# Kernel optimization log

Measured on AMD Instinct MI355X. Metric: run time of the kernel, lower is better.

The kernel has to match this reference:

```python
import math
import jax, jax.numpy as jnp
import numpy as np

B, CK, CV, T, H, W = 4, 512, 512, 3, 24, 24


def _conv(x, w, b):
    # 3x3, stride 1, pad 1 == SAME
    y = jax.lax.conv_general_dilated(x, w, (1, 1), 'SAME',
                                     dimension_numbers=('NCHW', 'OIHW', 'NCHW'))
    return y + b[None, :, None, None]


def _resblock(x, c1w, c1b, c2w, c2b, dsw=None, dsb=None):
    r = _conv(jax.nn.relu(x), c1w, c1b)
    r = _conv(jax.nn.relu(r), c2w, c2b)
    s = x if dsw is None else _conv(x, dsw, dsb)
    return s + r


def _up2(x):
    b, c, h, w = x.shape
    return jax.image.resize(x, (b, c, 2 * h, 2 * w), 'bilinear')


def _affinity(mk, qk):
    # mk: [B,CK,T,H,W], qk: [B,CK,H,W]
    b, ck = mk.shape[:2]
    mkf = mk.reshape(b, ck, -1)                       # [B,CK,THW]
    qkf = qk.reshape(b, ck, -1)                       # [B,CK,HW]
    a = jnp.sum(mkf * mkf, axis=1)[:, :, None]        # [B,THW,1]
    ab = 2.0 * jnp.einsum('bct,bcn->btn', mkf, qkf)   # [B,THW,HW]
    return jax.nn.softmax((-a + ab) / math.sqrt(ck), axis=1)


def _readout(aff, mv):
    b, cv, t, h, w = mv.shape
    mem = jnp.einsum('bct,btn->bcn', mv.reshape(b, cv, -1), aff)
    return mem.reshape(b, cv, h, w)


def _decoder(f16, f8, f4, p):
    x = _resblock(f16, p['cmp_c1_w'], p['cmp_c1_b'], p['cmp_c2_w'], p['cmp_c2_b'],
                  p['cmp_ds_w'], p['cmp_ds_b'])
    s = _conv(f8, p['u1_skip_w'], p['u1_skip_b']) + _up2(x)
    x = _resblock(s, p['u1_c1_w'], p['u1_c1_b'], p['u1_c2_w'], p['u1_c2_b'],
                  p['u1_ds_w'], p['u1_ds_b'])
    s = _conv(f4, p['u2_skip_w'], p['u2_skip_b']) + _up2(x)
    x = _resblock(s, p['u2_c1_w'], p['u2_c1_b'], p['u2_c2_w'], p['u2_c2_b'])
    x = _conv(jax.nn.relu(x), p['pred_w'], p['pred_b'])
    b, c, h, w = x.shape
    return jax.image.resize(x, (b, c, 4 * h, 4 * w), 'bilinear')


def setup_inputs():
    key = jax.random.key(0)
    ks = jax.random.split(key, 32)
    rn = lambda i, shape, s: jax.random.normal(ks[i], shape, jnp.float32) * s
    z = lambda n: jnp.zeros((n,), jnp.float32)
    return dict(
        qk16=rn(0, (B, CK, H, W), 1.0),
        qv16=rn(1, (B, 512, H, W), 1.0),
        qf8=rn(2, (B, 512, 2 * H, 2 * W), 1.0),
        qf4=rn(3, (B, 256, 4 * H, 4 * W), 1.0),
        mk16=rn(4, (B, CK, T, H, W), 1.0),
        mv16=rn(5, (B, CV, T, H, W), 1.0),
        firstk=rn(6, (B, CK, T, H, W), 1.0),
        firstv=rn(7, (B, CV, T, H, W), 1.0),
        adjk=rn(8, (B, CK, T, H, W), 1.0),
        adfv=rn(9, (B, CV, T, H, W), 1.0),
        mask_w=rn(10, (512, 1536, 3, 3), 0.02), mask_b=z(512),
        cmp_ds_w=rn(11, (512, 1024, 3, 3), 0.02), cmp_ds_b=z(512),
        cmp_c1_w=rn(12, (512, 1024, 3, 3), 0.02), cmp_c1_b=z(512),
        cmp_c2_w=rn(13, (512, 512, 3, 3), 0.02), cmp_c2_b=z(512),
        u1_skip_w=rn(14, (512, 512, 3, 3), 0.02), u1_skip_b=z(512),
        u1_ds_w=rn(15, (256, 512, 3, 3), 0.02), u1_ds_b=z(256),
        u1_c1_w=rn(16, (256, 512, 3, 3), 0.02), u1_c1_b=z(256),
        u1_c2_w=rn(17, (256, 256, 3, 3), 0.02), u1_c2_b=z(256),
        u2_skip_w=rn(18, (256, 256, 3, 3), 0.02), u2_skip_b=z(256),
        u2_c1_w=rn(19, (256, 256, 3, 3), 0.02), u2_c1_b=z(256),
        u2_c2_w=rn(20, (256, 256, 3, 3), 0.02), u2_c2_b=z(256),
        pred_w=rn(21, (1, 256, 3, 3), 0.02), pred_b=z(1),
    )


def reference(qk16, qv16, qf8, qf4, mk16, mv16, firstk, firstv, adjk, adfv,
              mask_w, mask_b, cmp_ds_w, cmp_ds_b, cmp_c1_w, cmp_c1_b,
              cmp_c2_w, cmp_c2_b, u1_skip_w, u1_skip_b, u1_ds_w, u1_ds_b,
              u1_c1_w, u1_c1_b, u1_c2_w, u1_c2_b, u2_skip_w, u2_skip_b,
              u2_c1_w, u2_c1_b, u2_c2_w, u2_c2_b, pred_w, pred_b):
    p = dict(mask_w=mask_w, mask_b=mask_b, cmp_ds_w=cmp_ds_w, cmp_ds_b=cmp_ds_b,
             cmp_c1_w=cmp_c1_w, cmp_c1_b=cmp_c1_b, cmp_c2_w=cmp_c2_w, cmp_c2_b=cmp_c2_b,
             u1_skip_w=u1_skip_w, u1_skip_b=u1_skip_b, u1_ds_w=u1_ds_w, u1_ds_b=u1_ds_b,
             u1_c1_w=u1_c1_w, u1_c1_b=u1_c1_b, u1_c2_w=u1_c2_w, u1_c2_b=u1_c2_b,
             u2_skip_w=u2_skip_w, u2_skip_b=u2_skip_b, u2_c1_w=u2_c1_w, u2_c1_b=u2_c1_b,
             u2_c2_w=u2_c2_w, u2_c2_b=u2_c2_b, pred_w=pred_w, pred_b=pred_b)
    # three affinity maps over the three memory banks
    afl = _affinity(mk16, qk16)
    afg = _affinity(firstk, qk16)
    afa = _affinity(adjk, qk16)
    locals_ = _readout(afl, mv16)
    globals_ = _readout(afg, firstv)
    adjs = _readout(afa, adfv)
    fusion = jnp.concatenate([locals_, globals_, adjs], axis=1)  # [B,1536,H,W]
    pool = jnp.mean(fusion, axis=(2, 3), keepdims=True)          # adaptive avg pool to 1x1
    m = jax.nn.sigmoid(_conv(fusion + pool, mask_w, mask_b))
    decodes = (locals_ * m + locals_) + (globals_ * m + globals_) + (adjs * m + adjs)
    decodes = jnp.concatenate([decodes, qv16], axis=1)           # [B,1024,H,W]
    logits = _decoder(decodes, qf8, qf4, p)                      # [B,1,16H,16W]
    prob = jax.nn.sigmoid(logits)
    # aggregate
    bg = jnp.prod(1.0 - prob, axis=1, keepdims=True)
    new_prob = jnp.clip(jnp.concatenate([bg, prob], axis=1), 1e-7, 1.0 - 1e-7)
    logits = jnp.log(new_prob / (1.0 - new_prob))                # [B,2,16H,16W]
    prob = jax.nn.softmax(logits, axis=1)[:, 1:]
    return logits, prob
```

## Files before the change

### kernel.cpp

```cpp
#include <hip/hip_runtime.h>
#include <math.h>


static constexpr int THW  = 1728;
static constexpr int HW16 = 576;

typedef __attribute__((ext_vector_type(8))) short bf16x8;
typedef __attribute__((ext_vector_type(4))) float f32x4;
typedef unsigned int uint;

__device__ __forceinline__ float sigmf(float x) { return 1.f / (1.f + expf(-x)); }

__device__ __forceinline__ float bf2f(unsigned short u) {
  union { float f; uint i; } x; x.i = ((uint)u) << 16; return x.f;
}
__device__ __forceinline__ unsigned short f2bf(float f) {
  union { float f; uint i; } x; x.f = f;
  uint r = x.i + 0x7fffu + ((x.i >> 16) & 1u);
  return (unsigned short)(r >> 16);
}
__device__ __forceinline__ uint relu2(uint x) {
  uint lo = (x & 0x8000u) ? 0u : (x & 0xFFFFu);
  uint hi = (x & 0x80000000u) ? 0u : (x & 0xFFFF0000u);
  return lo | hi;
}
__device__ __forceinline__ bf16x8 lds_ld8(const unsigned short* p) {
  union { uint2 u2[2]; bf16x8 v; } x;
  x.u2[0] = *(const uint2*)(p);
  x.u2[1] = *(const uint2*)(p + 4);
  return x.v;
}

__global__ __launch_bounds__(256) void tr_k(const float* __restrict__ in,
                                            unsigned short* __restrict__ out,
                                            int C, int HW) {
  __shared__ float t[32][33];
  int p0 = blockIdx.x << 5, c0 = blockIdx.y << 5, b = blockIdx.z;
  int tx = threadIdx.x & 31, ty = threadIdx.x >> 5;
  const float* ib = in + (size_t)b * C * HW;
  #pragma unroll
  for (int e = 0; e < 4; ++e)
    t[ty + e * 8][tx] = ib[(size_t)(c0 + ty + e * 8) * HW + p0 + tx];
  __syncthreads();
  unsigned short* ob = out + (size_t)b * C * HW;
  #pragma unroll
  for (int e = 0; e < 4; ++e)
    ob[(size_t)(p0 + ty + e * 8) * C + c0 + tx] = f2bf(t[tx][ty + e * 8]);
}

__global__ __launch_bounds__(256) void cvt_k(const float* __restrict__ in,
                                             unsigned short* __restrict__ o, int n) {
  int i = blockIdx.x * 256 + threadIdx.x;
  if (i < n) o[i] = f2bf(in[i]);
}

__global__ __launch_bounds__(256) void asq2_k(const unsigned short* __restrict__ mkT,
                                              float* __restrict__ asq) {
  int row = blockIdx.x * 4 + (threadIdx.x >> 6);
  int lane = threadIdx.x & 63;
  const unsigned short* p = mkT + (size_t)row * 512;
  float s = 0.f;
  #pragma unroll
  for (int i = 0; i < 8; ++i) { float v = bf2f(p[lane + (i << 6)]); s += v * v; }
  #pragma unroll
  for (int m = 32; m > 0; m >>= 1) s += __shfl_xor(s, m);
  if (lane == 0) asq[row] = s;
}

template<int EPI, int SPLIT>
__global__ __launch_bounds__(256) void mfgemm_k(
    const unsigned short* __restrict__ A, const unsigned short* __restrict__ Bm,
    float* __restrict__ C, const float* __restrict__ asq,
    int K, int ldc, int Nt, size_t aBS, size_t bBS, size_t cBS, float scale)
{
  const int by = blockIdx.y;
  const int b = by & 3, split = by >> 2;
  const int mt = blockIdx.x / Nt, nt = blockIdx.x - mt * Nt;
  const int m0 = mt << 6, n0 = nt << 6;
  const unsigned short* Ab = A + (size_t)b * aBS + (size_t)m0 * K;
  const unsigned short* Bb = Bm + (size_t)b * bBS + (size_t)n0 * K;
  __shared__ unsigned short sA[64][36];
  __shared__ unsigned short sB[64][36];
  const int tid = threadIdx.x;
  const int lane = tid & 63, wv = tid >> 6;
  const int mS = (wv >> 1) << 5, nS = (wv & 1) << 5;
  const int l15 = lane & 15, lq = lane >> 4;
  const int srow = tid >> 2, scol = (tid & 3) << 3;
  f32x4 acc[2][2];
  #pragma unroll
  for (int i = 0; i < 2; ++i)
    #pragma unroll
    for (int j = 0; j < 2; ++j) acc[i][j] = (f32x4){0.f, 0.f, 0.f, 0.f};
  const int Kper = K / SPLIT;
  const int kLo = split * Kper, kHi = kLo + Kper;
  for (int k0 = kLo; k0 < kHi; k0 += 32) {
    uint4 va = *(const uint4*)(Ab + (size_t)srow * K + k0 + scol);
    uint4 vb = *(const uint4*)(Bb + (size_t)srow * K + k0 + scol);
    *(uint2*)&sA[srow][scol]     = make_uint2(va.x, va.y);
    *(uint2*)&sA[srow][scol + 4] = make_uint2(va.z, va.w);
    *(uint2*)&sB[srow][scol]     = make_uint2(vb.x, vb.y);
    *(uint2*)&sB[srow][scol + 4] = make_uint2(vb.z, vb.w);
    __syncthreads();
    bf16x8 a0 = lds_ld8(&sA[mS + l15][lq << 3]);
    bf16x8 a1 = lds_ld8(&sA[mS + 16 + l15][lq << 3]);
    bf16x8 b0 = lds_ld8(&sB[nS + l15][lq << 3]);
    bf16x8 b1 = lds_ld8(&sB[nS + 16 + l15][lq << 3]);
    acc[0][0] = __builtin_amdgcn_mfma_f32_16x16x32_bf16(a0, b0, acc[0][0], 0, 0, 0);
    acc[0][1] = __builtin_amdgcn_mfma_f32_16x16x32_bf16(a0, b1, acc[0][1], 0, 0, 0);
    acc[1][0] = __builtin_amdgcn_mfma_f32_16x16x32_bf16(a1, b0, acc[1][0], 0, 0, 0);
    acc[1][1] = __builtin_amdgcn_mfma_f32_16x16x32_bf16(a1, b1, acc[1][1], 0, 0, 0);
    __syncthreads();
  }
  float* Cb = C + (size_t)(EPI == 2 ? (split * 4 + b) : b) * cBS;
  #pragma unroll
  for (int i = 0; i < 2; ++i) {
    const int mrow = m0 + mS + i * 16 + (lq << 2);
    #pragma unroll
    for (int j = 0; j < 2; ++j) {
      const int n = n0 + nS + j * 16 + l15;
      float4 v;
      if constexpr (EPI == 1) {
        float4 aq = *(const float4*)(asq + b * THW + mrow);
        v.x = (2.f * acc[i][j][0] - aq.x) * scale;
        v.y = (2.f * acc[i][j][1] - aq.y) * scale;
        v.z = (2.f * acc[i][j][2] - aq.z) * scale;
        v.w = (2.f * acc[i][j][3] - aq.w) * scale;
      } else {
        v.x = acc[i][j][0]; v.y = acc[i][j][1];
        v.z = acc[i][j][2]; v.w = acc[i][j][3];
      }
      *(float4*)(Cb + (size_t)n * ldc + mrow) = v;
    }
  }
}

__global__ __launch_bounds__(256) void softmaxT_k(const float* __restrict__ S,
                                                  unsigned short* __restrict__ P) {
  int row = blockIdx.x * 4 + (threadIdx.x >> 6);
  int lane = threadIdx.x & 63;
  const float* sp = S + (size_t)row * THW;
  float v[27];
  float mx = -3.0e38f;
  #pragma unroll
  for (int i = 0; i < 27; ++i) { v[i] = sp[lane + (i << 6)]; mx = fmaxf(mx, v[i]); }
  #pragma unroll
  for (int m = 32; m > 0; m >>= 1) mx = fmaxf(mx, __shfl_xor(mx, m));
  float sum = 0.f;
  #pragma unroll
  for (int i = 0; i < 27; ++i) { v[i] = expf(v[i] - mx); sum += v[i]; }
  #pragma unroll
  for (int m = 32; m > 0; m >>= 1) sum += __shfl_xor(sum, m);
  float inv = 1.f / sum;
  unsigned short* pp = P + (size_t)row * THW;
  #pragma unroll
  for (int i = 0; i < 27; ++i) pp[lane + (i << 6)] = f2bf(v[i] * inv);
}

__global__ __launch_bounds__(256) void skred3_k(const float* __restrict__ part,
                                                float* __restrict__ fusion, int cOff) {
  int i = blockIdx.x * 256 + threadIdx.x;
  if (i >= 4 * HW16 * 512) return;
  const int N = 4 * HW16 * 512;
  float v = part[i] + part[i + N] + part[i + 2 * N];
  int c = i & 511; int t = i >> 9; int n = t % HW16; int b = t / HW16;
  fusion[((size_t)b * HW16 + n) * 1536 + cOff + c] = v;
}

__global__ __launch_bounds__(128) void pool_k(const float* __restrict__ f,
                                              float* __restrict__ pool) {
  int b = blockIdx.y, c = blockIdx.x * 128 + threadIdx.x;
  const float* p = f + (size_t)b * HW16 * 1536 + c;
  float s = 0.f;
  for (int n = 0; n < HW16; ++n) s += p[(size_t)n * 1536];
  pool[b * 1536 + c] = s * (1.f / 576.f);
}

__global__ __launch_bounds__(256) void fusionp_k(const float* __restrict__ f,
                                                 const float* __restrict__ pool,
                                                 unsigned short* __restrict__ o, int total) {
  int i = blockIdx.x * 256 + threadIdx.x;
  if (i >= total) return;
  int c = i % 1536; int b = i / (HW16 * 1536);
  o[i] = f2bf(f[i] + pool[b * 1536 + c]);
}

__global__ __launch_bounds__(256) void decodes_k(const float* __restrict__ fusion,
                                                 const unsigned short* __restrict__ m,
                                                 const float* __restrict__ qv,
                                                 unsigned short* __restrict__ o) {
  int i = blockIdx.x * 256 + threadIdx.x;
  if (i >= 4 * HW16 * 1024) return;
  int c = i & 1023; int t = i >> 10; int n = t % HW16; int b = t / HW16;
  float v;
  if (c < 512) {
    const float* f = fusion + ((size_t)b * HW16 + n) * 1536;
    float s3 = f[c] + f[c + 512] + f[c + 1024];
    float mf = bf2f(m[((size_t)b * HW16 + n) * 512 + c]);
    v = s3 * (mf + 1.f);
  } else {
    v = qv[((size_t)b * 512 + (c - 512)) * HW16 + n];
  }
  o[i] = f2bf(v);
}

__global__ __launch_bounds__(256) void wrep_k(const float* __restrict__ w,
                                              unsigned short* __restrict__ o,
                                              int Cout, int Cin, int total) {
  int i = blockIdx.x * 256 + threadIdx.x;
  if (i >= total) return;
  int ci = i % Cin; int t = i / Cin; int co = t % Cout; int tap = t / Cout;
  o[i] = f2bf(w[((size_t)co * Cin + ci) * 9 + tap]);
}

template<bool RELU_IN, int ACT, bool SPLITK, bool HAS_ADD>
__global__ __launch_bounds__(256) void convmf_k(
    const unsigned short* __restrict__ in, const unsigned short* __restrict__ W2,
    const float* __restrict__ bias, const unsigned short* __restrict__ add,
    unsigned short* __restrict__ outb, float* __restrict__ outp,
    int Cin, int Cout, int H, int W, int ciPer)
{
  const int tilesX = W >> 3;
  const int tx0 = (blockIdx.x % tilesX) << 3;
  const int ty0 = (blockIdx.x / tilesX) << 3;
  const int co0 = blockIdx.y << 6;
  const int b = blockIdx.z & 3;
  const int split = blockIdx.z >> 2;
  const int HWp = H * W;
  __shared__ unsigned short sA[9][64][36];
  __shared__ unsigned short sB[100][36];
  const int tid = threadIdx.x;
  const int lane = tid & 63, wv = tid >> 6;
  const int cS = (wv >> 1) << 5;
  const int nS = (wv & 1) << 5;
  const int l15 = lane & 15, lq = lane >> 4;
  int hp0[2], gp[2];
  #pragma unroll
  for (int j = 0; j < 2; ++j) {
    int n = nS + j * 16 + l15;
    int py = n >> 3, px = n & 7;
    hp0[j] = py * 10 + px;
    gp[j] = (ty0 + py) * W + tx0 + px;
  }
  f32x4 acc[2][2];
  #pragma unroll
  for (int i = 0; i < 2; ++i)
    #pragma unroll
    for (int j = 0; j < 2; ++j) acc[i][j] = (f32x4){0.f, 0.f, 0.f, 0.f};
  const size_t inBase = (size_t)b * HWp * Cin;
  const int kLo = split * ciPer, kHi = kLo + ciPer;
  const int sco = tid >> 2;
  const int sc8 = (tid & 3) << 3;
  for (int k0 = kLo; k0 < kHi; k0 += 32) {
    #pragma unroll
    for (int tap = 0; tap < 9; ++tap) {
      const uint4 v = *(const uint4*)(W2 + ((size_t)(tap * Cout + co0 + sco) * Cin + k0 + sc8));
      *(uint2*)&sA[tap][sco][sc8]     = make_uint2(v.x, v.y);
      *(uint2*)&sA[tap][sco][sc8 + 4] = make_uint2(v.z, v.w);
    }
    #pragma unroll
    for (int e = 0; e < 2; ++e) {
      int idx = tid + (e << 8);
      if (idx < 400) {
        int hp = idx >> 2, c8 = (idx & 3) << 3;
        int hy = ty0 + (hp / 10) - 1;
        int hx = tx0 + (hp % 10) - 1;
        uint4 v = make_uint4(0u, 0u, 0u, 0u);
        if (hy >= 0 && hy < H && hx >= 0 && hx < W)
          v = *(const uint4*)(in + inBase + (size_t)(hy * W + hx) * Cin + k0 + c8);
        if (RELU_IN) { v.x = relu2(v.x); v.y = relu2(v.y); v.z = relu2(v.z); v.w = relu2(v.w); }
        *(uint2*)&sB[hp][c8]     = make_uint2(v.x, v.y);
        *(uint2*)&sB[hp][c8 + 4] = make_uint2(v.z, v.w);
      }
    }
    __syncthreads();
    const int DT[9] = {0, 1, 2, 10, 11, 12, 20, 21, 22};
    #pragma unroll
    for (int tap = 0; tap < 9; ++tap) {
      bf16x8 a0 = lds_ld8(&sA[tap][cS + l15][lq << 3]);
      bf16x8 a1 = lds_ld8(&sA[tap][cS + 16 + l15][lq << 3]);
      bf16x8 b0 = lds_ld8(&sB[hp0[0] + DT[tap]][lq << 3]);
      bf16x8 b1 = lds_ld8(&sB[hp0[1] + DT[tap]][lq << 3]);
      acc[0][0] = __builtin_amdgcn_mfma_f32_16x16x32_bf16(a0, b0, acc[0][0], 0, 0, 0);
      acc[0][1] = __builtin_amdgcn_mfma_f32_16x16x32_bf16(a0, b1, acc[0][1], 0, 0, 0);
      acc[1][0] = __builtin_amdgcn_mfma_f32_16x16x32_bf16(a1, b0, acc[1][0], 0, 0, 0);
      acc[1][1] = __builtin_amdgcn_mfma_f32_16x16x32_bf16(a1, b1, acc[1][1], 0, 0, 0);
    }
    __syncthreads();
  }
  #pragma unroll
  for (int i = 0; i < 2; ++i) {
    const int coB = co0 + cS + i * 16 + (lq << 2);
    #pragma unroll
    for (int j = 0; j < 2; ++j) {
      if constexpr (SPLITK) {
        float* dst = outp + ((size_t)(split * 4 + b) * HWp + gp[j]) * Cout + coB;
        float4 v; v.x = acc[i][j][0]; v.y = acc[i][j][1]; v.z = acc[i][j][2]; v.w = acc[i][j][3];
        *(float4*)dst = v;
      } else {
        float4 bv = *(const float4*)(bias + coB);
        float v0 = acc[i][j][0] + bv.x, v1 = acc[i][j][1] + bv.y;
        float v2 = acc[i][j][2] + bv.z, v3 = acc[i][j][3] + bv.w;
        const size_t base = ((size_t)b * HWp + gp[j]) * Cout + coB;
        if constexpr (HAS_ADD) {
          ushort4 a4 = *(const ushort4*)(add + base);
          v0 += bf2f(a4.x); v1 += bf2f(a4.y); v2 += bf2f(a4.z); v3 += bf2f(a4.w);
        }
        if constexpr (ACT == 1) { v0 = sigmf(v0); v1 = sigmf(v1); v2 = sigmf(v2); v3 = sigmf(v3); }
        ushort4 o; o.x = f2bf(v0); o.y = f2bf(v1); o.z = f2bf(v2); o.w = f2bf(v3);
        *(ushort4*)(outb + base) = o;
      }
    }
  }
}

template<int ACT, bool HAS_ADD>
__global__ __launch_bounds__(256) void skred_k(
    const float* __restrict__ part, const float* __restrict__ bias,
    const unsigned short* __restrict__ add, unsigned short* __restrict__ out,
    int Cout, int n)
{
  int i = blockIdx.x * 256 + threadIdx.x;
  if (i >= n) return;
  float v = part[i] + part[i + n] + bias[i % Cout];
  if (HAS_ADD) v += bf2f(add[i]);
  if (ACT == 1) v = sigmf(v);
  out[i] = f2bf(v);
}

__global__ __launch_bounds__(256) void up2add_k(unsigned short* __restrict__ s,
                                                const unsigned short* __restrict__ x,
                                                int OH, int OW, int C, int total) {
  int i = blockIdx.x * 256 + threadIdx.x;
  if (i >= total) return;
  int c = i % C; int op = i / C;
  int ox = op % OW; int t = op / OW; int oy = t % OH; int b = t / OH;
  int IH = OH >> 1, IW = OW >> 1;
  const unsigned short* xp = x + ((size_t)b * IH * IW) * C + c;
  float uy = 0.5f * oy - 0.25f;
  float ux = 0.5f * ox - 0.25f;
  int y0 = (int)floorf(uy); float fy = uy - (float)y0;
  int x0 = (int)floorf(ux); float fx = ux - (float)x0;
  int y0c = y0 < 0 ? 0 : y0; int y1c = (y0 + 1 >= IH) ? IH - 1 : y0 + 1;
  int x0c = x0 < 0 ? 0 : x0; int x1c = (x0 + 1 >= IW) ? IW - 1 : x0 + 1;
  float v00 = bf2f(xp[(size_t)(y0c * IW + x0c) * C]);
  float v01 = bf2f(xp[(size_t)(y0c * IW + x1c) * C]);
  float v10 = bf2f(xp[(size_t)(y1c * IW + x0c) * C]);
  float v11 = bf2f(xp[(size_t)(y1c * IW + x1c) * C]);
  float r = (1.f - fy) * ((1.f - fx) * v00 + fx * v01)
          + fy * ((1.f - fx) * v10 + fx * v11);
  s[i] = f2bf(bf2f(s[i]) + r);
}

__global__ __launch_bounds__(256) void pred_k(const unsigned short* __restrict__ in,
                                              const float* __restrict__ w,
                                              const float* __restrict__ bias,
                                              float* __restrict__ l4) {
  __shared__ float sw[9][256];
  for (int idx = threadIdx.x; idx < 2304; idx += 256)
    sw[idx % 9][idx / 9] = w[idx];
  __syncthreads();
  int gpix = blockIdx.x * 4 + (threadIdx.x >> 6);
  int b = gpix / 9216, pix = gpix % 9216;
  int py = pix / 96, px = pix % 96;
  int lane = threadIdx.x & 63;
  float acc = 0.f;
  #pragma unroll
  for (int ky = 0; ky < 3; ++ky) {
    int gy = py + ky - 1; if (gy < 0 || gy > 95) continue;
    #pragma unroll
    for (int kx = 0; kx < 3; ++kx) {
      int gx = px + kx - 1; if (gx < 0 || gx > 95) continue;
      const unsigned short* ip = in + ((size_t)b * 9216 + gy * 96 + gx) * 256;
      const float* wp = sw[ky * 3 + kx];
      #pragma unroll
      for (int cq = 0; cq < 4; ++cq) {
        int c = lane + (cq << 6);
        acc += fmaxf(bf2f(ip[c]), 0.f) * wp[c];
      }
    }
  }
  #pragma unroll
  for (int off = 32; off > 0; off >>= 1) acc += __shfl_down(acc, off);
  if (lane == 0) l4[gpix] = acc + bias[0];
}

__global__ __launch_bounds__(256) void final_k(const float* __restrict__ l4,
                                               float* __restrict__ out) {
  int i = blockIdx.x * 256 + threadIdx.x;
  if (i >= 4 * 384 * 384) return;
  int ox = i % 384; int t = i / 384; int oy = t % 384; int b = t / 384;
  const float* lp = l4 + (size_t)b * 96 * 96;
  float uy = 0.25f * oy - 0.375f;
  float ux = 0.25f * ox - 0.375f;
  int y0 = (int)floorf(uy); float fy = uy - (float)y0;
  int x0 = (int)floorf(ux); float fx = ux - (float)x0;
  int y0c = y0 < 0 ? 0 : y0; int y1c = (y0 + 1 > 95) ? 95 : y0 + 1;
  int x0c = x0 < 0 ? 0 : x0; int x1c = (x0 + 1 > 95) ? 95 : x0 + 1;
  float l = (1.f - fy) * ((1.f - fx) * lp[y0c * 96 + x0c] + fx * lp[y0c * 96 + x1c])
          + fy * ((1.f - fx) * lp[y1c * 96 + x0c] + fx * lp[y1c * 96 + x1c]);
  float p  = 1.f / (1.f + expf(-l));
  float p1 = fminf(fmaxf(p, 1e-7f), 1.f - 1e-7f);
  float p0 = fminf(fmaxf(1.f - p, 1e-7f), 1.f - 1e-7f);
  float L0 = logf(p0 / (1.f - p0));
  float L1 = logf(p1 / (1.f - p1));
  int sp = oy * 384 + ox;
  out[(size_t)(b * 2) * 147456 + sp] = L0;
  out[(size_t)(b * 2 + 1) * 147456 + sp] = L1;
  out[(size_t)1179648 + (size_t)b * 147456 + sp] = 1.f / (1.f + expf(L0 - L1));
}

extern "C" void kernel_launch(void* const* d_in, const int* in_sizes, int n_in,
                              void* d_out, int out_size, void* d_ws, size_t ws_size,
                              hipStream_t stream)
{
  (void)in_sizes; (void)n_in; (void)out_size; (void)ws_size;
  const float* qk16   = (const float*)d_in[0];
  const float* qv16   = (const float*)d_in[1];
  const float* qf8    = (const float*)d_in[2];
  const float* qf4    = (const float*)d_in[3];
  const float* mk16   = (const float*)d_in[4];
  const float* mv16   = (const float*)d_in[5];
  const float* firstk = (const float*)d_in[6];
  const float* firstv = (const float*)d_in[7];
  const float* adjk   = (const float*)d_in[8];
  const float* adfv   = (const float*)d_in[9];
  const float* mask_w   = (const float*)d_in[10];
  const float* mask_b   = (const float*)d_in[11];
  const float* cmp_ds_w = (const float*)d_in[12];
  const float* cmp_ds_b = (const float*)d_in[13];
  const float* cmp_c1_w = (const float*)d_in[14];
  const float* cmp_c1_b = (const float*)d_in[15];
  const float* cmp_c2_w = (const float*)d_in[16];
  const float* cmp_c2_b = (const float*)d_in[17];
  const float* u1_skip_w = (const float*)d_in[18];
  const float* u1_skip_b = (const float*)d_in[19];
  const float* u1_ds_w   = (const float*)d_in[20];
  const float* u1_ds_b   = (const float*)d_in[21];
  const float* u1_c1_w   = (const float*)d_in[22];
  const float* u1_c1_b   = (const float*)d_in[23];
  const float* u1_c2_w   = (const float*)d_in[24];
  const float* u1_c2_b   = (const float*)d_in[25];
  const float* u2_skip_w = (const float*)d_in[26];
  const float* u2_skip_b = (const float*)d_in[27];
  const float* u2_c1_w   = (const float*)d_in[28];
  const float* u2_c1_b   = (const float*)d_in[29];
  const float* u2_c2_w   = (const float*)d_in[30];
  const float* u2_c2_b   = (const float*)d_in[31];
  const float* pred_w    = (const float*)d_in[32];
  const float* pred_b    = (const float*)d_in[33];
  float* out = (float*)d_out;

  char* wsb = (char*)d_ws;
  unsigned short* Wsl = (unsigned short*)(wsb);
  char* slA = wsb + 23592960;
  char* slB = wsb + 42467328;
  char* slC = wsb + 61341696;
  char* slD = wsb + 70778880;
  char* slE = wsb + 80216064;
  char* slF = wsb + 84934656;
  char* slG = wsb + 89653248;
  char* slS = wsb + 92012544;

  unsigned short* mkT = Wsl;
  unsigned short* mvb = Wsl + 3538944;
  unsigned short* qkT = Wsl + 7077888;
  float* aff      = (float*)slA;
  float* rpart    = (float*)slA;
  unsigned short* Pmat = (unsigned short*)slC;
  float* fusion   = (float*)slB;
  float* partial  = (float*)slC;
  unsigned short* qf8t    = (unsigned short*)slC;
  unsigned short* x8      = (unsigned short*)slC;
  unsigned short* fusionp = (unsigned short*)slD;
  unsigned short* s8      = (unsigned short*)slD;
  unsigned short* dec     = (unsigned short*)slE;
  unsigned short* t1_8    = (unsigned short*)slE;
  unsigned short* t1      = (unsigned short*)slF;
  unsigned short* t2      = (unsigned short*)(slF + 2359296);
  unsigned short* t2_8    = (unsigned short*)slF;
  unsigned short* mbuf    = (unsigned short*)slG;
  unsigned short* x16     = (unsigned short*)slG;
  unsigned short* qf4t    = (unsigned short*)slA;
  unsigned short* t1_4    = (unsigned short*)slA;
  unsigned short* s4      = (unsigned short*)slB;
  float* asqb   = (float*)slS;
  float* poolb  = (float*)(slS + 36864);
  float* l4     = (float*)(slS + 61440);

  const float scale = 0.04419417382415922f;

  tr_k<<<dim3(18, 16, 4), 256, 0, stream>>>(qk16, qkT, 512, 576);
  const float* banksK[3] = {mk16, firstk, adjk};
  const float* banksV[3] = {mv16, firstv, adfv};
  for (int bank = 0; bank < 3; ++bank) {
    tr_k<<<dim3(54, 16, 4), 256, 0, stream>>>(banksK[bank], mkT, 512, 1728);
    asq2_k<<<1728, 256, 0, stream>>>(mkT, asqb);
    mfgemm_k<1, 1><<<dim3(243, 4), 256, 0, stream>>>(
        mkT, qkT, aff, asqb, 512, THW, 9,
        (size_t)THW * 512, (size_t)HW16 * 512, (size_t)HW16 * THW, scale);
    softmaxT_k<<<576, 256, 0, stream>>>(aff, Pmat);
    cvt_k<<<(3538944 + 255) / 256, 256, 0, stream>>>(banksV[bank], mvb, 3538944);
    mfgemm_k<2, 3><<<dim3(72, 12), 256, 0, stream>>>(
        mvb, Pmat, rpart, nullptr, 1728, 512, 9,
        (size_t)512 * THW, (size_t)HW16 * THW, (size_t)HW16 * 512, 0.f);
    skred3_k<<<(1179648 + 255) / 256, 256, 0, stream>>>(rpart, fusion, bank * 512);
  }

  pool_k<<<dim3(12, 4), 128, 0, stream>>>(fusion, poolb);
  fusionp_k<<<(3538944 + 255) / 256, 256, 0, stream>>>(fusion, poolb, fusionp, 3538944);

  wrep_k<<<(7077888 + 255) / 256, 256, 0, stream>>>(mask_w, Wsl, 512, 1536, 7077888);
  convmf_k<false, 0, true, false><<<dim3(9, 8, 8), 256, 0, stream>>>(
      fusionp, Wsl, nullptr, nullptr, nullptr, partial, 1536, 512, 24, 24, 768);
  skred_k<1, false><<<(1179648 + 255) / 256, 256, 0, stream>>>(
      partial, mask_b, nullptr, mbuf, 512, 1179648);

  decodes_k<<<(2359296 + 255) / 256, 256, 0, stream>>>(fusion, mbuf, qv16, dec);

  wrep_k<<<(4718592 + 255) / 256, 256, 0, stream>>>(cmp_c1_w, Wsl, 512, 1024, 4718592);
  wrep_k<<<(2359296 + 255) / 256, 256, 0, stream>>>(cmp_c2_w, Wsl + 4718592, 512, 512, 2359296);
  wrep_k<<<(4718592 + 255) / 256, 256, 0, stream>>>(cmp_ds_w, Wsl + 7077888, 512, 1024, 4718592);
  convmf_k<true, 0, true, false><<<dim3(9, 8, 8), 256, 0, stream>>>(
      dec, Wsl, nullptr, nullptr, nullptr, partial, 1024, 512, 24, 24, 512);
  skred_k<0, false><<<(1179648 + 255) / 256, 256, 0, stream>>>(
      partial, cmp_c1_b, nullptr, t1, 512, 1179648);
  convmf_k<true, 0, true, false><<<dim3(9, 8, 8), 256, 0, stream>>>(
      t1, Wsl + 4718592, nullptr, nullptr, nullptr, partial, 512, 512, 24, 24, 256);
  skred_k<0, false><<<(1179648 + 255) / 256, 256, 0, stream>>>(
      partial, cmp_c2_b, nullptr, t2, 512, 1179648);
  convmf_k<false, 0, true, false><<<dim3(9, 8, 8), 256, 0, stream>>>(
      dec, Wsl + 7077888, nullptr, nullptr, nullptr, partial, 1024, 512, 24, 24, 512);
  skred_k<0, true><<<(1179648 + 255) / 256, 256, 0, stream>>>(
      partial, cmp_ds_b, t2, x16, 512, 1179648);

  tr_k<<<dim3(72, 16, 4), 256, 0, stream>>>(qf8, qf8t, 512, 2304);
  wrep_k<<<(2359296 + 255) / 256, 256, 0, stream>>>(u1_skip_w, Wsl, 512, 512, 2359296);
  wrep_k<<<(1179648 + 255) / 256, 256, 0, stream>>>(u1_c1_w, Wsl + 2359296, 256, 512, 1179648);
  wrep_k<<<(589824 + 255) / 256, 256, 0, stream>>>(u1_c2_w, Wsl + 3538944, 256, 256, 589824);
  wrep_k<<<(1179648 + 255) / 256, 256, 0, stream>>>(u1_ds_w, Wsl + 4128768, 256, 512, 1179648);
  convmf_k<false, 0, false, false><<<dim3(36, 8, 4), 256, 0, stream>>>(
      qf8t, Wsl, u1_skip_b, nullptr, s8, nullptr, 512, 512, 48, 48, 512);
  up2add_k<<<(4718592 + 255) / 256, 256, 0, stream>>>(s8, x16, 48, 48, 512, 4718592);
  convmf_k<true, 0, false, false><<<dim3(36, 4, 4), 256, 0, stream>>>(
      s8, Wsl + 2359296, u1_c1_b, nullptr, t1_8, nullptr, 512, 256, 48, 48, 512);
  convmf_k<true, 0, false, false><<<dim3(36, 4, 4), 256, 0, stream>>>(
      t1_8, Wsl + 3538944, u1_c2_b, nullptr, t2_8, nullptr, 256, 256, 48, 48, 256);
  convmf_k<false, 0, false, true><<<dim3(36, 4, 4), 256, 0, stream>>>(
      s8, Wsl + 4128768, u1_ds_b, t2_8, x8, nullptr, 512, 256, 48, 48, 512);

  tr_k<<<dim3(288, 8, 4), 256, 0, stream>>>(qf4, qf4t, 256, 9216);
  wrep_k<<<(589824 + 255) / 256, 256, 0, stream>>>(u2_skip_w, Wsl, 256, 256, 589824);
  wrep_k<<<(589824 + 255) / 256, 256, 0, stream>>>(u2_c1_w, Wsl + 589824, 256, 256, 589824);
  wrep_k<<<(589824 + 255) / 256, 256, 0, stream>>>(u2_c2_w, Wsl + 1179648, 256, 256, 589824);
  convmf_k<false, 0, false, false><<<dim3(144, 4, 4), 256, 0, stream>>>(
      qf4t, Wsl, u2_skip_b, nullptr, s4, nullptr, 256, 256, 96, 96, 256);
  up2add_k<<<(9437184 + 255) / 256, 256, 0, stream>>>(s4, x8, 96, 96, 256, 9437184);
  convmf_k<true, 0, false, false><<<dim3(144, 4, 4), 256, 0, stream>>>(
      s4, Wsl + 589824, u2_c1_b, nullptr, t1_4, nullptr, 256, 256, 96, 96, 256);
  convmf_k<true, 0, false, true><<<dim3(144, 4, 4), 256, 0, stream>>>(
      t1_4, Wsl + 1179648, u2_c2_b, s4, s4, nullptr, 256, 256, 96, 96, 256);

  pred_k<<<9216, 256, 0, stream>>>(s4, pred_w, pred_b, l4);
  final_k<<<(589824 + 255) / 256, 256, 0, stream>>>(l4, out);
}
```

Measured before the change: 1.490 ms.

## Enlarge conv MFMA tiles to 128x128 with per-row weight staging and more split-K

Replaces the 64-channel by 8x8-pixel conv tile with a 128-channel by 16x8-pixel tile. Each wave now holds a 4x4 block of MFMA accumulators, and the weights are staged one kernel row (3 taps) at a time. The tile edge is clamped so a 48-wide image (not a multiple of 16) still fits. The LDS row stride becomes 40 so reads and writes can use 16-byte accesses, and the GEMM kernel gets the same padding. Split-K is raised to 4 on the 24x24 convs and added as 2-way on the 48x48 convs so the grid stays full with fewer blocks. The price is more reduction passes over fp32 partials, higher register pressure from 64 accumulator floats per lane, and overlapping writes at the clamped tile edge.

New measurement: 1.310 ms. -12.0%, faster.

```diff
diff --git a/kernel.cpp b/kernel.cpp
--- a/kernel.cpp
+++ b/kernel.cpp
@@ -25,9 +25,8 @@
   return lo | hi;
 }
 __device__ __forceinline__ bf16x8 lds_ld8(const unsigned short* p) {
-  union { uint2 u2[2]; bf16x8 v; } x;
-  x.u2[0] = *(const uint2*)(p);
-  x.u2[1] = *(const uint2*)(p + 4);
+  union { uint4 u4; bf16x8 v; } x;
+  x.u4 = *(const uint4*)(p);
   return x.v;
 }
 
@@ -79,8 +78,8 @@
   const int m0 = mt << 6, n0 = nt << 6;
   const unsigned short* Ab = A + (size_t)b * aBS + (size_t)m0 * K;
   const unsigned short* Bb = Bm + (size_t)b * bBS + (size_t)n0 * K;
-  __shared__ unsigned short sA[64][36];
-  __shared__ unsigned short sB[64][36];
+  __shared__ unsigned short sA[64][40];
+  __shared__ unsigned short sB[64][40];
   const int tid = threadIdx.x;
   const int lane = tid & 63, wv = tid >> 6;
   const int mS = (wv >> 1) << 5, nS = (wv & 1) << 5;
@@ -96,10 +95,8 @@
   for (int k0 = kLo; k0 < kHi; k0 += 32) {
     uint4 va = *(const uint4*)(Ab + (size_t)srow * K + k0 + scol);
     uint4 vb = *(const uint4*)(Bb + (size_t)srow * K + k0 + scol);
-    *(uint2*)&sA[srow][scol]     = make_uint2(va.x, va.y);
-    *(uint2*)&sA[srow][scol + 4] = make_uint2(va.z, va.w);
-    *(uint2*)&sB[srow][scol]     = make_uint2(vb.x, vb.y);
-    *(uint2*)&sB[srow][scol + 4] = make_uint2(vb.z, vb.w);
+    *(uint4*)&sA[srow][scol] = va;
+    *(uint4*)&sB[srow][scol] = vb;
     __syncthreads();
     bf16x8 a0 = lds_ld8(&sA[mS + l15][lq << 3]);
     bf16x8 a1 = lds_ld8(&sA[mS + 16 + l15][lq << 3]);
@@ -213,85 +210,94 @@
 }
 
 template<bool RELU_IN, int ACT, bool SPLITK, bool HAS_ADD>
-__global__ __launch_bounds__(256) void convmf_k(
+__global__ __launch_bounds__(256) void convmf2_k(
     const unsigned short* __restrict__ in, const unsigned short* __restrict__ W2,
     const float* __restrict__ bias, const unsigned short* __restrict__ add,
     unsigned short* __restrict__ outb, float* __restrict__ outp,
     int Cin, int Cout, int H, int W, int ciPer)
 {
-  const int tilesX = W >> 3;
-  const int tx0 = (blockIdx.x % tilesX) << 3;
-  const int ty0 = (blockIdx.x / tilesX) << 3;
-  const int co0 = blockIdx.y << 6;
+  const int xT = (W + 15) >> 4;
+  const int xt = blockIdx.x % xT, yt = blockIdx.x / xT;
+  int tx0 = xt << 4; if (tx0 > W - 16) tx0 = W - 16;
+  const int ty0 = yt << 3;
+  const int co0 = blockIdx.y << 7;
   const int b = blockIdx.z & 3;
   const int split = blockIdx.z >> 2;
   const int HWp = H * W;
-  __shared__ unsigned short sA[9][64][36];
-  __shared__ unsigned short sB[100][36];
+  __shared__ unsigned short sA[3][128][40];
+  __shared__ unsigned short sB[180][40];
   const int tid = threadIdx.x;
   const int lane = tid & 63, wv = tid >> 6;
-  const int cS = (wv >> 1) << 5;
-  const int nS = (wv & 1) << 5;
+  const int coQ = (wv >> 1) << 6;
+  const int nQ  = (wv & 1) << 6;
   const int l15 = lane & 15, lq = lane >> 4;
-  int hp0[2], gp[2];
-  #pragma unroll
-  for (int j = 0; j < 2; ++j) {
-    int n = nS + j * 16 + l15;
-    int py = n >> 3, px = n & 7;
-    hp0[j] = py * 10 + px;
+  int rowb[4], gp[4];
+  #pragma unroll
+  for (int j = 0; j < 4; ++j) {
+    int n = nQ + 16 * j + l15;
+    int py = n >> 4, px = n & 15;
+    rowb[j] = py * 18 + px;
     gp[j] = (ty0 + py) * W + tx0 + px;
   }
-  f32x4 acc[2][2];
-  #pragma unroll
-  for (int i = 0; i < 2; ++i)
+  f32x4 acc[4][4];
+  #pragma unroll
+  for (int i = 0; i < 4; ++i)
     #pragma unroll
-    for (int j = 0; j < 2; ++j) acc[i][j] = (f32x4){0.f, 0.f, 0.f, 0.f};
+    for (int j = 0; j < 4; ++j) acc[i][j] = (f32x4){0.f, 0.f, 0.f, 0.f};
   const size_t inBase = (size_t)b * HWp * Cin;
   const int kLo = split * ciPer, kHi = kLo + ciPer;
-  const int sco = tid >> 2;
-  const int sc8 = (tid & 3) << 3;
   for (int k0 = kLo; k0 < kHi; k0 += 32) {
     #pragma unroll
-    for (int tap = 0; tap < 9; ++tap) {
-      const uint4 v = *(const uint4*)(W2 + ((size_t)(tap * Cout + co0 + sco) * Cin + k0 + sc8));
-      *(uint2*)&sA[tap][sco][sc8]     = make_uint2(v.x, v.y);
-      *(uint2*)&sA[tap][sco][sc8 + 4] = make_uint2(v.z, v.w);
-    }
-    #pragma unroll
-    for (int e = 0; e < 2; ++e) {
-      int idx = tid + (e << 8);
-      if (idx < 400) {
-        int hp = idx >> 2, c8 = (idx & 3) << 3;
-        int hy = ty0 + (hp / 10) - 1;
-        int hx = tx0 + (hp % 10) - 1;
-        uint4 v = make_uint4(0u, 0u, 0u, 0u);
-        if (hy >= 0 && hy < H && hx >= 0 && hx < W)
-          v = *(const uint4*)(in + inBase + (size_t)(hy * W + hx) * Cin + k0 + c8);
-        if (RELU_IN) { v.x = relu2(v.x); v.y = relu2(v.y); v.z = relu2(v.z); v.w = relu2(v.w); }
-        *(uint2*)&sB[hp][c8]     = make_uint2(v.x, v.y);
-        *(uint2*)&sB[hp][c8 + 4] = make_uint2(v.z, v.w);
+    for (int ky = 0; ky < 3; ++ky) {
+      __syncthreads();
+      if (ky == 0) {
+        #pragma unroll
+        for (int e = 0; e < 3; ++e) {
+          int idx = tid + (e << 8);
+          if (idx < 720) {
+            int hp = idx >> 2, c8 = (idx & 3) << 3;
+            int hy = ty0 + hp / 18 - 1;
+            int hx = tx0 + hp % 18 - 1;
+            uint4 v = make_uint4(0u, 0u, 0u, 0u);
+            if (hy >= 0 && hy < H && hx >= 0 && hx < W)
+              v = *(const uint4*)(in + inBase + (size_t)(hy * W + hx) * Cin + k0 + c8);
+            if (RELU_IN) { v.x = relu2(v.x); v.y = relu2(v.y); v.z = relu2(v.z); v.w = relu2(v.w); }
+            *(uint4*)&sB[hp][c8] = v;
+          }
+        }
+      }
+      #pragma unroll
+      for (int e = 0; e < 6; ++e) {
+        int idx = tid + (e << 8);
+        int kx = idx >> 9;
+        int rem = idx & 511;
+        int co = rem >> 2, c8 = (rem & 3) << 3;
+        uint4 v = *(const uint4*)(W2 + ((size_t)((ky * 3 + kx) * Cout + co0 + co) * Cin + k0 + c8));
+        *(uint4*)&sA[kx][co][c8] = v;
+      }
+      __syncthreads();
+      #pragma unroll
+      for (int kx = 0; kx < 3; ++kx) {
+        bf16x8 a[4], bb[4];
+        #pragma unroll
+        for (int i = 0; i < 4; ++i)
+          a[i] = lds_ld8(&sA[kx][coQ + 16 * i + l15][lq << 3]);
+        #pragma unroll
+        for (int j = 0; j < 4; ++j)
+          bb[j] = lds_ld8(&sB[rowb[j] + ky * 18 + kx][lq << 3]);
+        #pragma unroll
+        for (int i = 0; i < 4; ++i)
+          #pragma unroll
+          for (int j = 0; j < 4; ++j)
+            acc[i][j] = __builtin_amdgcn_mfma_f32_16x16x32_bf16(a[i], bb[j], acc[i][j], 0, 0, 0);
       }
     }
-    __syncthreads();
-    const int DT[9] = {0, 1, 2, 10, 11, 12, 20, 21, 22};
+  }
+  #pragma unroll
+  for (int i = 0; i < 4; ++i) {
+    const int coB = co0 + coQ + 16 * i + (lq << 2);
     #pragma unroll
-    for (int tap = 0; tap < 9; ++tap) {
-      bf16x8 a0 = lds_ld8(&sA[tap][cS + l15][lq << 3]);
-      bf16x8 a1 = lds_ld8(&sA[tap][cS + 16 + l15][lq << 3]);
-      bf16x8 b0 = lds_ld8(&sB[hp0[0] + DT[tap]][lq << 3]);
-      bf16x8 b1 = lds_ld8(&sB[hp0[1] + DT[tap]][lq << 3]);
-      acc[0][0] = __builtin_amdgcn_mfma_f32_16x16x32_bf16(a0, b0, acc[0][0], 0, 0, 0);
-      acc[0][1] = __builtin_amdgcn_mfma_f32_16x16x32_bf16(a0, b1, acc[0][1], 0, 0, 0);
-      acc[1][0] = __builtin_amdgcn_mfma_f32_16x16x32_bf16(a1, b0, acc[1][0], 0, 0, 0);
-      acc[1][1] = __builtin_amdgcn_mfma_f32_16x16x32_bf16(a1, b1, acc[1][1], 0, 0, 0);
-    }
-    __syncthreads();
-  }
-  #pragma unroll
-  for (int i = 0; i < 2; ++i) {
-    const int coB = co0 + cS + i * 16 + (lq << 2);
-    #pragma unroll
-    for (int j = 0; j < 2; ++j) {
+    for (int j = 0; j < 4; ++j) {
       if constexpr (SPLITK) {
         float* dst = outp + ((size_t)(split * 4 + b) * HWp + gp[j]) * Cout + coB;
         float4 v; v.x = acc[i][j][0]; v.y = acc[i][j][1]; v.z = acc[i][j][2]; v.w = acc[i][j][3];
@@ -313,7 +319,7 @@
   }
 }
 
-template<int ACT, bool HAS_ADD>
+template<int NS, int ACT, bool HAS_ADD>
 __global__ __launch_bounds__(256) void skred_k(
     const float* __restrict__ part, const float* __restrict__ bias,
     const unsigned short* __restrict__ add, unsigned short* __restrict__ out,
@@ -321,7 +327,9 @@
 {
   int i = blockIdx.x * 256 + threadIdx.x;
   if (i >= n) return;
-  float v = part[i] + part[i + n] + bias[i % Cout];
+  float v = bias[i % Cout];
+  #pragma unroll
+  for (int s = 0; s < NS; ++s) v += part[i + (size_t)s * n];
   if (HAS_ADD) v += bf2f(add[i]);
   if (ACT == 1) v = sigmf(v);
   out[i] = f2bf(v);
@@ -468,7 +476,7 @@
   float* rpart    = (float*)slA;
   unsigned short* Pmat = (unsigned short*)slC;
   float* fusion   = (float*)slB;
-  float* partial  = (float*)slC;
+  float* partial  = (float*)slA;
   unsigned short* qf8t    = (unsigned short*)slC;
   unsigned short* x8      = (unsigned short*)slC;
   unsigned short* fusionp = (unsigned short*)slD;
@@ -510,9 +518,9 @@
   fusionp_k<<<(3538944 + 255) / 256, 256, 0, stream>>>(fusion, poolb, fusionp, 3538944);
 
   wrep_k<<<(7077888 + 255) / 256, 256, 0, stream>>>(mask_w, Wsl, 512, 1536, 7077888);
-  convmf_k<false, 0, true, false><<<dim3(9, 8, 8), 256, 0, stream>>>(
-      fusionp, Wsl, nullptr, nullptr, nullptr, partial, 1536, 512, 24, 24, 768);
-  skred_k<1, false><<<(1179648 + 255) / 256, 256, 0, stream>>>(
+  convmf2_k<false, 0, true, false><<<dim3(6, 4, 16), 256, 0, stream>>>(
+      fusionp, Wsl, nullptr, nullptr, nullptr, partial, 1536, 512, 24, 24, 384);
+  skred_k<4, 1, false><<<(1179648 + 255) / 256, 256, 0, stream>>>(
       partial, mask_b, nullptr, mbuf, 512, 1179648);
 
   decodes_k<<<(2359296 + 255) / 256, 256, 0, stream>>>(fusion, mbuf, qv16, dec);
@@ -520,17 +528,17 @@
   wrep_k<<<(4718592 + 255) / 256, 256, 0, stream>>>(cmp_c1_w, Wsl, 512, 1024, 4718592);
   wrep_k<<<(2359296 + 255) / 256, 256, 0, stream>>>(cmp_c2_w, Wsl + 4718592, 512, 512, 2359296);
   wrep_k<<<(4718592 + 255) / 256, 256, 0, stream>>>(cmp_ds_w, Wsl + 7077888, 512, 1024, 4718592);
-  convmf_k<true, 0, true, false><<<dim3(9, 8, 8), 256, 0, stream>>>(
-      dec, Wsl, nullptr, nullptr, nullptr, partial, 1024, 512, 24, 24, 512);
-  skred_k<0, false><<<(1179648 + 255) / 256, 256, 0, stream>>>(
+  convmf2_k<true, 0, true, false><<<dim3(6, 4, 16), 256, 0, stream>>>(
+      dec, Wsl, nullptr, nullptr, nullptr, partial, 1024, 512, 24, 24, 256);
+  skred_k<4, 0, false><<<(1179648 + 255) / 256, 256, 0, stream>>>(
       partial, cmp_c1_b, nullptr, t1, 512, 1179648);
-  convmf_k<true, 0, true, false><<<dim3(9, 8, 8), 256, 0, stream>>>(
-      t1, Wsl + 4718592, nullptr, nullptr, nullptr, partial, 512, 512, 24, 24, 256);
-  skred_k<0, false><<<(1179648 + 255) / 256, 256, 0, stream>>>(
+  convmf2_k<true, 0, true, false><<<dim3(6, 4, 16), 256, 0, stream>>>(
+      t1, Wsl + 4718592, nullptr, nullptr, nullptr, partial, 512, 512, 24, 24, 128);
+  skred_k<4, 0, false><<<(1179648 + 255) / 256, 256, 0, stream>>>(
       partial, cmp_c2_b, nullptr, t2, 512, 1179648);
-  convmf_k<false, 0, true, false><<<dim3(9, 8, 8), 256, 0, stream>>>(
-      dec, Wsl + 7077888, nullptr, nullptr, nullptr, partial, 1024, 512, 24, 24, 512);
-  skred_k<0, true><<<(1179648 + 255) / 256, 256, 0, stream>>>(
+  convmf2_k<false, 0, true, false><<<dim3(6, 4, 16), 256, 0, stream>>>(
+      dec, Wsl + 7077888, nullptr, nullptr, nullptr, partial, 1024, 512, 24, 24, 256);
+  skred_k<4, 0, true><<<(1179648 + 255) / 256, 256, 0, stream>>>(
       partial, cmp_ds_b, t2, x16, 512, 1179648);
 
   tr_k<<<dim3(72, 16, 4), 256, 0, stream>>>(qf8, qf8t, 512, 2304);
@@ -538,26 +546,32 @@
   wrep_k<<<(1179648 + 255) / 256, 256, 0, stream>>>(u1_c1_w, Wsl + 2359296, 256, 512, 1179648);
   wrep_k<<<(589824 + 255) / 256, 256, 0, stream>>>(u1_c2_w, Wsl + 3538944, 256, 256, 589824);
   wrep_k<<<(1179648 + 255) / 256, 256, 0, stream>>>(u1_ds_w, Wsl + 4128768, 256, 512, 1179648);
-  convmf_k<false, 0, false, false><<<dim3(36, 8, 4), 256, 0, stream>>>(
+  convmf2_k<false, 0, false, false><<<dim3(18, 4, 4), 256, 0, stream>>>(
       qf8t, Wsl, u1_skip_b, nullptr, s8, nullptr, 512, 512, 48, 48, 512);
   up2add_k<<<(4718592 + 255) / 256, 256, 0, stream>>>(s8, x16, 48, 48, 512, 4718592);
-  convmf_k<true, 0, false, false><<<dim3(36, 4, 4), 256, 0, stream>>>(
-      s8, Wsl + 2359296, u1_c1_b, nullptr, t1_8, nullptr, 512, 256, 48, 48, 512);
-  convmf_k<true, 0, false, false><<<dim3(36, 4, 4), 256, 0, stream>>>(
-      t1_8, Wsl + 3538944, u1_c2_b, nullptr, t2_8, nullptr, 256, 256, 48, 48, 256);
-  convmf_k<false, 0, false, true><<<dim3(36, 4, 4), 256, 0, stream>>>(
-      s8, Wsl + 4128768, u1_ds_b, t2_8, x8, nullptr, 512, 256, 48, 48, 512);
+  convmf2_k<true, 0, true, false><<<dim3(18, 2, 8), 256, 0, stream>>>(
+      s8, Wsl + 2359296, nullptr, nullptr, nullptr, partial, 512, 256, 48, 48, 256);
+  skred_k<2, 0, false><<<(2359296 + 255) / 256, 256, 0, stream>>>(
+      partial, u1_c1_b, nullptr, t1_8, 256, 2359296);
+  convmf2_k<true, 0, true, false><<<dim3(18, 2, 8), 256, 0, stream>>>(
+      t1_8, Wsl + 3538944, nullptr, nullptr, nullptr, partial, 256, 256, 48, 48, 128);
+  skred_k<2, 0, false><<<(2359296 + 255) / 256, 256, 0, stream>>>(
+      partial, u1_c2_b, nullptr, t2_8, 256, 2359296);
+  convmf2_k<false, 0, true, false><<<dim3(18, 2, 8), 256, 0, stream>>>(
+      s8, Wsl + 4128768, nullptr, nullptr, nullptr, partial, 512, 256, 48, 48, 256);
+  skred_k<2, 0, true><<<(2359296 + 255) / 256, 256, 0, stream>>>(
+      partial, u1_ds_b, t2_8, x8, 256, 2359296);
 
   tr_k<<<dim3(288, 8, 4), 256, 0, stream>>>(qf4, qf4t, 256, 9216);
   wrep_k<<<(589824 + 255) / 256, 256, 0, stream>>>(u2_skip_w, Wsl, 256, 256, 589824);
   wrep_k<<<(589824 + 255) / 256, 256, 0, stream>>>(u2_c1_w, Wsl + 589824, 256, 256, 589824);
   wrep_k<<<(589824 + 255) / 256, 256, 0, stream>>>(u2_c2_w, Wsl + 1179648, 256, 256, 589824);
-  convmf_k<false, 0, false, false><<<dim3(144, 4, 4), 256, 0, stream>>>(
+  convmf2_k<false, 0, false, false><<<dim3(72, 2, 4), 256, 0, stream>>>(
       qf4t, Wsl, u2_skip_b, nullptr, s4, nullptr, 256, 256, 96, 96, 256);
   up2add_k<<<(9437184 + 255) / 256, 256, 0, stream>>>(s4, x8, 96, 96, 256, 9437184);
-  convmf_k<true, 0, false, false><<<dim3(144, 4, 4), 256, 0, stream>>>(
+  convmf2_k<true, 0, false, false><<<dim3(72, 2, 4), 256, 0, stream>>>(
       s4, Wsl + 589824, u2_c1_b, nullptr, t1_4, nullptr, 256, 256, 96, 96, 256);
-  convmf_k<true, 0, false, true><<<dim3(144, 4, 4), 256, 0, stream>>>(
+  convmf2_k<true, 0, false, true><<<dim3(72, 2, 4), 256, 0, stream>>>(
       t1_4, Wsl + 1179648, u2_c2_b, s4, s4, nullptr, 256, 256, 96, 96, 256);
 
   pred_k<<<9216, 256, 0, stream>>>(s4, pred_w, pred_b, l4);
```
